# Optimization experiments

Hardware: AMD Instinct MI355X
Metric: run time of the kernel (lower is better)

The kernel has to match this reference:

```python
import jax, jax.numpy as jnp
import numpy as np

N_NODES = 20000
N_EDGES = 200000
NODE_DIM = 32
EDGE_DIM = 16
HIDDEN = 32
N_GRAPHS = 64


def setup_inputs() -> dict:
    key = jax.random.key(0)
    ks = jax.random.split(key, 20)
    x = jax.random.normal(ks[0], (N_NODES, NODE_DIM), jnp.float32)
    edge_attr = jax.random.normal(ks[1], (N_EDGES, EDGE_DIM), jnp.float32)
    edge_index = jax.random.randint(ks[2], (2, N_EDGES), 0, N_NODES, jnp.int64)
    batch = jnp.sort(jax.random.randint(ks[3], (N_NODES,), 0, N_GRAPHS, jnp.int64))
    s = 0.1
    # conv1 edge network: EDGE_DIM -> HIDDEN -> NODE_DIM*HIDDEN
    en1_W1 = jax.random.normal(ks[4], (EDGE_DIM, HIDDEN), jnp.float32) * s
    en1_b1 = jnp.zeros((HIDDEN,), jnp.float32)
    en1_W2 = jax.random.normal(ks[5], (HIDDEN, NODE_DIM * HIDDEN), jnp.float32) * s
    en1_b2 = jnp.zeros((NODE_DIM * HIDDEN,), jnp.float32)
    root1 = jax.random.normal(ks[6], (NODE_DIM, HIDDEN), jnp.float32) * s
    bias1 = jnp.zeros((HIDDEN,), jnp.float32)
    # conv2 edge network: EDGE_DIM -> HIDDEN -> HIDDEN*HIDDEN
    en2_W1 = jax.random.normal(ks[7], (EDGE_DIM, HIDDEN), jnp.float32) * s
    en2_b1 = jnp.zeros((HIDDEN,), jnp.float32)
    en2_W2 = jax.random.normal(ks[8], (HIDDEN, HIDDEN * HIDDEN), jnp.float32) * s
    en2_b2 = jnp.zeros((HIDDEN * HIDDEN,), jnp.float32)
    root2 = jax.random.normal(ks[9], (HIDDEN, HIDDEN), jnp.float32) * s
    bias2 = jnp.zeros((HIDDEN,), jnp.float32)
    # output head
    fc_W = jax.random.normal(ks[10], (HIDDEN, 2), jnp.float32) * s
    fc_b = jnp.zeros((2,), jnp.float32)
    return {
        "x": x, "edge_attr": edge_attr, "edge_index": edge_index, "batch": batch,
        "en1_W1": en1_W1, "en1_b1": en1_b1, "en1_W2": en1_W2, "en1_b2": en1_b2,
        "root1": root1, "bias1": bias1,
        "en2_W1": en2_W1, "en2_b1": en2_b1, "en2_W2": en2_W2, "en2_b2": en2_b2,
        "root2": root2, "bias2": bias2,
        "fc_W": fc_W, "fc_b": fc_b,
    }


def _segment_mean(vals, ids, num_segments):
    s = jax.ops.segment_sum(vals, ids, num_segments=num_segments)
    cnt = jax.ops.segment_sum(jnp.ones((vals.shape[0],), vals.dtype), ids, num_segments=num_segments)
    return s / jnp.maximum(cnt, 1.0)[:, None]


def _nnconv(x, src, tgt, edge_attr, W1, b1, W2, b2, root, bias, in_c, out_c, n_nodes):
    # edge MLP -> per-edge weight matrix [E, in_c, out_c]
    h = jax.nn.relu(edge_attr @ W1 + b1)
    Wedge = (h @ W2 + b2).reshape(-1, in_c, out_c)
    # gather source feats, per-edge matvec, scatter-mean to targets
    msg = jnp.einsum('ei,eio->eo', x[src], Wedge)
    agg = _segment_mean(msg, tgt, n_nodes)
    return agg + x @ root + bias


def reference(x, edge_attr, edge_index, batch,
              en1_W1, en1_b1, en1_W2, en1_b2, root1, bias1,
              en2_W1, en2_b1, en2_W2, en2_b2, root2, bias2,
              fc_W, fc_b):
    src, tgt = edge_index[0], edge_index[1]
    h = _nnconv(x, src, tgt, edge_attr, en1_W1, en1_b1, en1_W2, en1_b2,
                root1, bias1, NODE_DIM, HIDDEN, N_NODES)
    h = jax.nn.relu(h)
    h = _nnconv(h, src, tgt, edge_attr, en2_W1, en2_b1, en2_W2, en2_b2,
                root2, bias2, HIDDEN, HIDDEN, N_NODES)
    h = jax.nn.relu(h)
    g = _segment_mean(h, batch, N_GRAPHS)  # global_mean_pool
    return g @ fc_W + fc_b
```

## Files before the change

### kernel.cpp

```cpp
#include <hip/hip_runtime.h>

#define N_NODES   20000
#define N_EDGES   200000
#define NODE_DIM  32
#define EDGE_DIM  16
#define HIDDEN    32
#define N_GRAPHS  64
#define T_NODES   14


__global__ __launch_bounds__(256) void build_deg2_kernel(
    const int* __restrict__ tgts, const int* __restrict__ srcs,
    int* __restrict__ deg_t, int* __restrict__ deg_s)
{
    int e = blockIdx.x * blockDim.x + threadIdx.x;
    if (e >= N_EDGES) return;
    atomicAdd(deg_t + tgts[e], 1);
    atomicAdd(deg_s + srcs[e], 1);
}

__device__ void chunked_scan(const int* __restrict__ deg, int* __restrict__ start,
                             int* __restrict__ cursor, int* partial)
{
    const int C = (N_NODES + 255) / 256;
    int t  = threadIdx.x;
    int lo = t * C;
    int hi = lo + C < N_NODES ? lo + C : N_NODES;
    int s = 0;
    for (int i = lo; i < hi; ++i) s += deg[i];
    partial[t] = s;
    __syncthreads();
    if (t == 0) {
        int run = 0;
        for (int i = 0; i < 256; ++i) { int v = partial[i]; partial[i] = run; run += v; }
    }
    __syncthreads();
    int run = partial[t];
    for (int i = lo; i < hi; ++i) {
        start[i]  = run;
        cursor[i] = run;
        run += deg[i];
    }
    if (lo < N_NODES && hi == N_NODES) start[N_NODES] = run;
    __syncthreads();
}

__global__ __launch_bounds__(256) void scan2_kernel(
    const int* __restrict__ deg_t, int* __restrict__ start_t, int* __restrict__ cur_t,
    const int* __restrict__ deg_s, int* __restrict__ start_s, int* __restrict__ cur_s)
{
    __shared__ int partial[256];
    chunked_scan(deg_t, start_t, cur_t, partial);
    chunked_scan(deg_s, start_s, cur_s, partial);
}

__global__ __launch_bounds__(256) void scatter2_kernel(
    const int* __restrict__ tgts, const int* __restrict__ srcs,
    int* __restrict__ cur_t, int* __restrict__ cur_s,
    int* __restrict__ pos_t, int* __restrict__ eid_s)
{
    int e = blockIdx.x * blockDim.x + threadIdx.x;
    if (e >= N_EDGES) return;
    int p1 = atomicAdd(cur_t + tgts[e], 1);
    pos_t[e] = p1;
    int p2 = atomicAdd(cur_s + srcs[e], 1);
    eid_s[p2] = e;
}

__global__ __launch_bounds__(256, 2) void src_conv_kernel(
    const float* __restrict__ feat,
    const float* __restrict__ ea,
    const int*   __restrict__ srcs,
    const int*   __restrict__ start_s,
    const int*   __restrict__ eid_s,
    const int*   __restrict__ pos_t,
    const float* __restrict__ W1,
    const float* __restrict__ b1,
    const float* __restrict__ W2,
    const float* __restrict__ b2,
    float*       __restrict__ msg)
{
    __shared__ __align__(16) float P[T_NODES][1024];
    __shared__ __align__(16) float Q[T_NODES][32];
    __shared__ __align__(16) float XT[T_NODES][32];
    __shared__ __align__(16) float Hs[8][32];

    int tid = threadIdx.x;
    int v0  = blockIdx.x * T_NODES;
    int T_act = (N_NODES - v0) < T_NODES ? (N_NODES - v0) : T_NODES;

    if (tid < 8 * T_NODES) {
        int t  = tid >> 3;
        int og = tid & 7;
        int vv = v0 + t; if (vv > N_NODES - 1) vv = N_NODES - 1;
        float4 xx = *reinterpret_cast<const float4*>(feat + (size_t)vv * 32 + og * 4);
        *reinterpret_cast<float4*>(&XT[t][og * 4]) = xx;
    }
    __syncthreads();

    {
        int og = tid & 7;
        int k  = tid >> 3;
        float acc[T_NODES][4];
        #pragma unroll
        for (int t = 0; t < T_NODES; ++t) {
            acc[t][0] = 0.f; acc[t][1] = 0.f; acc[t][2] = 0.f; acc[t][3] = 0.f;
        }
        const float* w2p = W2 + (size_t)k * 1024 + og * 4;
        #pragma unroll
        for (int i = 0; i < 32; ++i) {
            float4 w4 = *reinterpret_cast<const float4*>(w2p + i * 32);
            #pragma unroll
            for (int t = 0; t < T_NODES; ++t) {
                float xv = XT[t][i];
                acc[t][0] += xv * w4.x; acc[t][1] += xv * w4.y;
                acc[t][2] += xv * w4.z; acc[t][3] += xv * w4.w;
            }
        }
        #pragma unroll
        for (int t = 0; t < T_NODES; ++t) {
            #pragma unroll
            for (int c = 0; c < 4; ++c) {
                int o = og * 4 + c;
                P[t][o * 32 + (k ^ ((o & 7) << 2))] = acc[t][c];
            }
        }
    }
    if (tid < 8 * T_NODES) {
        int t  = tid >> 3;
        int og = tid & 7;
        float q0 = 0.f, q1 = 0.f, q2 = 0.f, q3 = 0.f;
        const float* b2p = b2 + og * 4;
        #pragma unroll
        for (int i = 0; i < 32; ++i) {
            float4 b4 = *reinterpret_cast<const float4*>(b2p + i * 32);
            float xv = XT[t][i];
            q0 += xv * b4.x; q1 += xv * b4.y; q2 += xv * b4.z; q3 += xv * b4.w;
        }
        float4 qq; qq.x = q0; qq.y = q1; qq.z = q2; qq.w = q3;
        *reinterpret_cast<float4*>(&Q[t][og * 4]) = qq;
    }
    __syncthreads();

    int jb = start_s[v0];
    int je = start_s[v0 + T_act];
    int slot = tid >> 5;
    int kl   = tid & 31;
    int sw   = (kl & 7) << 2;

    float w1c[EDGE_DIM];
    #pragma unroll
    for (int j = 0; j < EDGE_DIM; ++j) w1c[j] = W1[j * 32 + kl];
    float b1v = b1[kl];

    for (int j0 = jb; j0 < je; j0 += 8) {
        int j = j0 + slot;
        if (j < je) {
            int e  = eid_s[j];
            int sl = srcs[e] - v0;
            int pr = pos_t[e];
            const float4* ea4 = reinterpret_cast<const float4*>(ea + (size_t)e * EDGE_DIM);
            float4 a0 = ea4[0], a1 = ea4[1], a2 = ea4[2], a3 = ea4[3];
            float hv = b1v;
            hv += a0.x * w1c[0]  + a0.y * w1c[1]  + a0.z * w1c[2]  + a0.w * w1c[3];
            hv += a1.x * w1c[4]  + a1.y * w1c[5]  + a1.z * w1c[6]  + a1.w * w1c[7];
            hv += a2.x * w1c[8]  + a2.y * w1c[9]  + a2.z * w1c[10] + a2.w * w1c[11];
            hv += a3.x * w1c[12] + a3.y * w1c[13] + a3.z * w1c[14] + a3.w * w1c[15];
            Hs[slot][kl] = fmaxf(hv, 0.f);

            float accv = Q[sl][kl];
            const float* Pt = &P[sl][kl * 32];
            #pragma unroll
            for (int kq = 0; kq < 32; kq += 4) {
                float4 hq = *reinterpret_cast<const float4*>(&Hs[slot][kq]);
                float4 pq = *reinterpret_cast<const float4*>(&Pt[kq ^ sw]);
                accv += hq.x * pq.x + hq.y * pq.y + hq.z * pq.z + hq.w * pq.w;
            }
            msg[(size_t)pr * 32 + kl] = accv;
        }
    }
}

__global__ __launch_bounds__(256, 2) void gather_update_kernel(
    const float* __restrict__ feat,
    const float* __restrict__ msg,
    const int*   __restrict__ start,
    const float* __restrict__ root,
    const float* __restrict__ bias,
    float*       __restrict__ outf,
    const int*   __restrict__ batch,
    float*       __restrict__ pool,
    float*       __restrict__ pcnt)
{
    int idx = blockIdx.x * blockDim.x + threadIdx.x;
    int v  = idx >> 3;
    int c4 = idx & 7;
    if (v >= N_NODES) return;

    int s0 = start[v], s1 = start[v + 1];
    const float4* m4 = reinterpret_cast<const float4*>(msg);

    float4 a0 = {0.f,0.f,0.f,0.f}, a1 = {0.f,0.f,0.f,0.f};
    float4 a2 = {0.f,0.f,0.f,0.f}, a3 = {0.f,0.f,0.f,0.f};
    int j = s0;
    for (; j + 4 <= s1; j += 4) {
        float4 t0 = m4[(size_t)(j + 0) * 8 + c4];
        float4 t1 = m4[(size_t)(j + 1) * 8 + c4];
        float4 t2 = m4[(size_t)(j + 2) * 8 + c4];
        float4 t3 = m4[(size_t)(j + 3) * 8 + c4];
        a0.x += t0.x; a0.y += t0.y; a0.z += t0.z; a0.w += t0.w;
        a1.x += t1.x; a1.y += t1.y; a1.z += t1.z; a1.w += t1.w;
        a2.x += t2.x; a2.y += t2.y; a2.z += t2.z; a2.w += t2.w;
        a3.x += t3.x; a3.y += t3.y; a3.z += t3.z; a3.w += t3.w;
    }
    for (; j < s1; ++j) {
        float4 t = m4[(size_t)j * 8 + c4];
        a0.x += t.x; a0.y += t.y; a0.z += t.z; a0.w += t.w;
    }
    float sx = (a0.x + a1.x) + (a2.x + a3.x);
    float sy = (a0.y + a1.y) + (a2.y + a3.y);
    float sz = (a0.z + a1.z) + (a2.z + a3.z);
    float sw_ = (a0.w + a1.w) + (a2.w + a3.w);

    int d = s1 - s0;
    float invd = 1.0f / (float)(d > 0 ? d : 1);
    float4 bb = *reinterpret_cast<const float4*>(bias + c4 * 4);
    float ax = sx * invd + bb.x;
    float ay = sy * invd + bb.y;
    float az = sz * invd + bb.z;
    float aw = sw_ * invd + bb.w;

    const float*  xv = feat + (size_t)v * 32;
    const float4* r4 = reinterpret_cast<const float4*>(root);
    #pragma unroll
    for (int i = 0; i < 32; ++i) {
        float  xi = xv[i];
        float4 rr = r4[i * 8 + c4];
        ax += xi * rr.x; ay += xi * rr.y; az += xi * rr.z; aw += xi * rr.w;
    }
    ax = fmaxf(ax, 0.f); ay = fmaxf(ay, 0.f); az = fmaxf(az, 0.f); aw = fmaxf(aw, 0.f);

    if (outf) {
        float4 t; t.x = ax; t.y = ay; t.z = az; t.w = aw;
        *reinterpret_cast<float4*>(outf + (size_t)v * 32 + c4 * 4) = t;
    }
    if (batch) {
        int g = batch[v];
        float* p = pool + (size_t)g * 32 + c4 * 4;
        atomicAdd(p + 0, ax); atomicAdd(p + 1, ay);
        atomicAdd(p + 2, az); atomicAdd(p + 3, aw);
        if (c4 == 0) atomicAdd(pcnt + g, 1.0f);
    }
}

__global__ void head_kernel(
    const float* __restrict__ pool, const float* __restrict__ pcnt,
    const float* __restrict__ fcW, const float* __restrict__ fcb,
    float* __restrict__ out)
{
    int g = threadIdx.x;
    if (g >= N_GRAPHS) return;
    float inv = 1.0f / fmaxf(pcnt[g], 1.0f);
    float o0 = fcb[0], o1 = fcb[1];
    #pragma unroll
    for (int i = 0; i < 32; ++i) {
        float m = pool[g * 32 + i] * inv;
        o0 += m * fcW[i * 2 + 0];
        o1 += m * fcW[i * 2 + 1];
    }
    out[g * 2 + 0] = o0;
    out[g * 2 + 1] = o1;
}

__global__ __launch_bounds__(256) void build_deg_kernel(
    const int* __restrict__ tgts, int* __restrict__ deg)
{
    int e = blockIdx.x * blockDim.x + threadIdx.x;
    if (e >= N_EDGES) return;
    atomicAdd(deg + tgts[e], 1);
}

__global__ __launch_bounds__(256) void scan_deg_kernel(
    const int* __restrict__ deg, int* __restrict__ start, int* __restrict__ cursor)
{
    __shared__ int partial[256];
    chunked_scan(deg, start, cursor, partial);
}

__global__ __launch_bounds__(256) void scatter_edges_kernel(
    const int* __restrict__ tgts, int* __restrict__ cursor, int* __restrict__ eid)
{
    int e = blockIdx.x * blockDim.x + threadIdx.x;
    if (e >= N_EDGES) return;
    int pos = atomicAdd(cursor + tgts[e], 1);
    eid[pos] = e;
}

__global__ __launch_bounds__(256) void edge_msg_kernel(
    const float* __restrict__ feat, const float* __restrict__ ea,
    const int* __restrict__ srcs,
    const float* __restrict__ W1, const float* __restrict__ b1,
    const float* __restrict__ W2, const float* __restrict__ b2,
    float* __restrict__ msg)
{
    int e = blockIdx.x * blockDim.x + threadIdx.x;
    if (e >= N_EDGES) return;
    float a[EDGE_DIM];
    const float4* ea4 = reinterpret_cast<const float4*>(ea + (size_t)e * EDGE_DIM);
    #pragma unroll
    for (int q = 0; q < EDGE_DIM / 4; ++q) {
        float4 t = ea4[q];
        a[q*4+0] = t.x; a[q*4+1] = t.y; a[q*4+2] = t.z; a[q*4+3] = t.w;
    }
    int s = srcs[e];
    float x[32];
    const float4* x4 = reinterpret_cast<const float4*>(feat + (size_t)s * 32);
    #pragma unroll
    for (int q = 0; q < 8; ++q) {
        float4 t = x4[q];
        x[q*4+0] = t.x; x[q*4+1] = t.y; x[q*4+2] = t.z; x[q*4+3] = t.w;
    }
    float acc[32];
    #pragma unroll
    for (int o = 0; o < 32; ++o) acc[o] = 0.0f;
    #pragma unroll
    for (int i = 0; i < 32; ++i) {
        float xi = x[i];
        #pragma unroll
        for (int o = 0; o < 32; ++o) acc[o] += xi * b2[i*32+o];
    }
    for (int k = 0; k < 32; ++k) {
        float hk = b1[k];
        #pragma unroll
        for (int j = 0; j < EDGE_DIM; ++j) hk += a[j] * W1[j*32 + k];
        hk = fmaxf(hk, 0.0f);
        const float* w = W2 + (size_t)k * 1024;
        #pragma unroll
        for (int i = 0; i < 32; ++i) {
            float c = hk * x[i];
            #pragma unroll
            for (int o = 0; o < 32; ++o) acc[o] += c * w[i*32+o];
        }
    }
    float4* m4 = reinterpret_cast<float4*>(msg + (size_t)e * 32);
    #pragma unroll
    for (int q = 0; q < 8; ++q) {
        float4 t;
        t.x = acc[q*4+0]; t.y = acc[q*4+1]; t.z = acc[q*4+2]; t.w = acc[q*4+3];
        m4[q] = t;
    }
}

__global__ __launch_bounds__(256) void gather_update_eid_kernel(
    const float* __restrict__ feat, const float* __restrict__ msg,
    const int* __restrict__ start, const int* __restrict__ eid,
    const float* __restrict__ root, const float* __restrict__ bias,
    float* __restrict__ outf, const int* __restrict__ batch,
    float* __restrict__ pool, float* __restrict__ pcnt)
{
    int idx = blockIdx.x * blockDim.x + threadIdx.x;
    int v = idx >> 5;
    int o = idx & 31;
    if (v >= N_NODES) return;
    int s0 = start[v], s1 = start[v + 1];
    float sum = 0.0f;
    for (int j = s0; j < s1; ++j) {
        int e = eid[j];
        sum += msg[(size_t)e * 32 + o];
    }
    int d = s1 - s0;
    float acc = sum / (float)(d > 0 ? d : 1) + bias[o];
    const float* xv = feat + (size_t)v * 32;
    #pragma unroll
    for (int i = 0; i < 32; ++i) acc += xv[i] * root[i * 32 + o];
    acc = fmaxf(acc, 0.0f);
    if (outf) outf[(size_t)v * 32 + o] = acc;
    if (batch) {
        int g = batch[v];
        atomicAdd(pool + (size_t)g * 32 + o, acc);
        if (o == 0) atomicAdd(pcnt + g, 1.0f);
    }
}


extern "C" void kernel_launch(void* const* d_in, const int* in_sizes, int n_in,
                              void* d_out, int out_size, void* d_ws, size_t ws_size,
                              hipStream_t stream)
{
    const float* x      = (const float*)d_in[0];
    const float* ea     = (const float*)d_in[1];
    const int*   ei     = (const int*)d_in[2];
    const int*   batch  = (const int*)d_in[3];
    const float* en1_W1 = (const float*)d_in[4];
    const float* en1_b1 = (const float*)d_in[5];
    const float* en1_W2 = (const float*)d_in[6];
    const float* en1_b2 = (const float*)d_in[7];
    const float* root1  = (const float*)d_in[8];
    const float* bias1  = (const float*)d_in[9];
    const float* en2_W1 = (const float*)d_in[10];
    const float* en2_b1 = (const float*)d_in[11];
    const float* en2_W2 = (const float*)d_in[12];
    const float* en2_b2 = (const float*)d_in[13];
    const float* root2  = (const float*)d_in[14];
    const float* bias2  = (const float*)d_in[15];
    const float* fcW    = (const float*)d_in[16];
    const float* fcb    = (const float*)d_in[17];

    const int* srcs = ei;
    const int* tgts = ei + N_EDGES;

    dim3 eb(256), eg((N_EDGES + 255) / 256);
    dim3 gb(256), gg((N_NODES * 8 + 255) / 256);
    const int NBLK = (N_NODES + T_NODES - 1) / T_NODES;

    size_t need_new = (size_t)2*N_NODES + N_GRAPHS*32 + N_GRAPHS
                    + 2*(N_NODES + 2) + 2*N_NODES + 2*(size_t)N_EDGES
                    + (size_t)N_EDGES*32 + (size_t)N_NODES*32;

    if (ws_size >= need_new * sizeof(float)) {
        int*   deg_t   = (int*)d_ws;
        int*   deg_s   = deg_t + N_NODES;
        float* pool    = (float*)(deg_s + N_NODES);
        float* pcnt    = pool + (size_t)N_GRAPHS*32;
        int*   start_t = (int*)(pcnt + N_GRAPHS);
        int*   cur_t   = start_t + (N_NODES + 2);
        int*   pos_t   = cur_t + N_NODES;
        int*   start_s = pos_t + N_EDGES;
        int*   cur_s   = start_s + (N_NODES + 2);
        int*   eid_s   = cur_s + N_NODES;
        float* msg     = (float*)(eid_s + N_EDGES);
        float* h1      = msg + (size_t)N_EDGES*32;
        size_t zeroBytes = ((size_t)2*N_NODES + N_GRAPHS*32 + N_GRAPHS) * sizeof(float);

        hipMemsetAsync(d_ws, 0, zeroBytes, stream);

        build_deg2_kernel<<<eg, eb, 0, stream>>>(tgts, srcs, deg_t, deg_s);
        scan2_kernel<<<dim3(1), dim3(256), 0, stream>>>(deg_t, start_t, cur_t,
                                                        deg_s, start_s, cur_s);
        scatter2_kernel<<<eg, eb, 0, stream>>>(tgts, srcs, cur_t, cur_s, pos_t, eid_s);

        src_conv_kernel<<<dim3(NBLK), dim3(256), 0, stream>>>(
            x, ea, srcs, start_s, eid_s, pos_t, en1_W1, en1_b1, en1_W2, en1_b2, msg);
        gather_update_kernel<<<gg, gb, 0, stream>>>(x, msg, start_t, root1, bias1,
                                                    h1, nullptr, nullptr, nullptr);
        src_conv_kernel<<<dim3(NBLK), dim3(256), 0, stream>>>(
            h1, ea, srcs, start_s, eid_s, pos_t, en2_W1, en2_b1, en2_W2, en2_b2, msg);
        gather_update_kernel<<<gg, gb, 0, stream>>>(h1, msg, start_t, root2, bias2,
                                                    nullptr, batch, pool, pcnt);

        head_kernel<<<dim3(1), dim3(64), 0, stream>>>(pool, pcnt, fcW, fcb, (float*)d_out);
    } else {
        int*   deg    = (int*)d_ws;
        float* pool   = (float*)(deg + N_NODES);
        float* pcnt   = pool + (size_t)N_GRAPHS*32;
        int*   start  = (int*)(pcnt + N_GRAPHS);
        int*   cursor = start + (N_NODES + 1);
        int*   eid    = cursor + N_NODES;
        float* msg    = (float*)(eid + N_EDGES);
        float* h1     = msg + (size_t)N_EDGES*32;
        size_t zeroBytes = ((size_t)N_NODES + N_GRAPHS*32 + N_GRAPHS) * sizeof(float);

        hipMemsetAsync(d_ws, 0, zeroBytes, stream);

        dim3 gg32((N_NODES * 32 + 255) / 256);
        build_deg_kernel<<<eg, eb, 0, stream>>>(tgts, deg);
        scan_deg_kernel<<<dim3(1), dim3(256), 0, stream>>>(deg, start, cursor);
        scatter_edges_kernel<<<eg, eb, 0, stream>>>(tgts, cursor, eid);

        edge_msg_kernel<<<eg, eb, 0, stream>>>(x, ea, srcs,
                                               en1_W1, en1_b1, en1_W2, en1_b2, msg);
        gather_update_eid_kernel<<<gg32, gb, 0, stream>>>(x, msg, start, eid, root1, bias1,
                                                          h1, nullptr, nullptr, nullptr);
        edge_msg_kernel<<<eg, eb, 0, stream>>>(h1, ea, srcs,
                                               en2_W1, en2_b1, en2_W2, en2_b2, msg);
        edge_msg_kernel<<<eg, eb, 0, stream>>>(h1, ea, srcs,
                                               en2_W1, en2_b1, en2_W2, en2_b2, msg);
        gather_update_eid_kernel<<<gg32, gb, 0, stream>>>(h1, msg, start, eid, root2, bias2,
                                                          nullptr, batch, pool, pcnt);
        head_kernel<<<dim3(1), dim3(64), 0, stream>>>(pool, pcnt, fcW, fcb, (float*)d_out);
    }
}
```

Before: 446.3 us.

## Balance the gather by edge-count blocks with shared-memory binning of messages

Replaces the per-node gather/update with an edge-balanced scheme. Blocks own a fixed span of target-sorted message rows, find their node range by binary search over start offsets, and accumulate rows into shared-memory bins with LDS atomics. Each row also records its target node in a new mapping array. The goal is to remove load imbalance from skewed in-degrees and to give coalesced row reads. The cost is an extra kernel, extra workspace, shared atomics and an uncoalesced per-thread root matvec.

Measured after the change: 508.4 us. 13.9% more time.

```diff
diff --git a/kernel.cpp b/kernel.cpp
--- a/kernel.cpp
+++ b/kernel.cpp
@@ -7,6 +7,9 @@
 #define HIDDEN    32
 #define N_GRAPHS  64
 #define T_NODES   14
+#define R_PER_BLK 512
+#define NCHUNK    128
+#define NB_GATHER ((N_EDGES + R_PER_BLK - 1) / R_PER_BLK)
 
 
 __global__ __launch_bounds__(256) void build_deg2_kernel(
@@ -57,28 +60,40 @@
 __global__ __launch_bounds__(256) void scatter2_kernel(
     const int* __restrict__ tgts, const int* __restrict__ srcs,
     int* __restrict__ cur_t, int* __restrict__ cur_s,
-    int* __restrict__ pos_t, int* __restrict__ eid_s)
+    int* __restrict__ pos_t, int* __restrict__ eid_s, int* __restrict__ r2n)
 {
     int e = blockIdx.x * blockDim.x + threadIdx.x;
     if (e >= N_EDGES) return;
-    int p1 = atomicAdd(cur_t + tgts[e], 1);
+    int t = tgts[e];
+    int p1 = atomicAdd(cur_t + t, 1);
     pos_t[e] = p1;
+    r2n[p1]  = t;
     int p2 = atomicAdd(cur_s + srcs[e], 1);
     eid_s[p2] = e;
 }
 
+__global__ __launch_bounds__(256) void find_block_starts_kernel(
+    const int* __restrict__ start_t, int* __restrict__ blk_first)
+{
+    int b = blockIdx.x * blockDim.x + threadIdx.x;
+    if (b > NB_GATHER) return;
+    int target = b * R_PER_BLK;
+    int lo = 0, hi = N_NODES + 1;
+    while (lo < hi) {
+        int mid = (lo + hi) >> 1;
+        if (start_t[mid] < target) lo = mid + 1; else hi = mid;
+    }
+    if (lo > N_NODES) lo = N_NODES;
+    blk_first[b] = lo;
+}
+
 __global__ __launch_bounds__(256, 2) void src_conv_kernel(
-    const float* __restrict__ feat,
-    const float* __restrict__ ea,
-    const int*   __restrict__ srcs,
-    const int*   __restrict__ start_s,
-    const int*   __restrict__ eid_s,
-    const int*   __restrict__ pos_t,
-    const float* __restrict__ W1,
-    const float* __restrict__ b1,
-    const float* __restrict__ W2,
-    const float* __restrict__ b2,
-    float*       __restrict__ msg)
+    const float* __restrict__ feat, const float* __restrict__ ea,
+    const int* __restrict__ srcs, const int* __restrict__ start_s,
+    const int* __restrict__ eid_s, const int* __restrict__ pos_t,
+    const float* __restrict__ W1, const float* __restrict__ b1,
+    const float* __restrict__ W2, const float* __restrict__ b2,
+    float* __restrict__ msg)
 {
     __shared__ __align__(16) float P[T_NODES][1024];
     __shared__ __align__(16) float Q[T_NODES][32];
@@ -181,10 +196,12 @@
     }
 }
 
-__global__ __launch_bounds__(256, 2) void gather_update_kernel(
+__global__ __launch_bounds__(256) void gather_block_kernel(
     const float* __restrict__ feat,
     const float* __restrict__ msg,
-    const int*   __restrict__ start,
+    const int*   __restrict__ start_t,
+    const int*   __restrict__ r2n,
+    const int*   __restrict__ blk_first,
     const float* __restrict__ root,
     const float* __restrict__ bias,
     float*       __restrict__ outf,
@@ -192,16 +209,93 @@
     float*       __restrict__ pool,
     float*       __restrict__ pcnt)
 {
+    __shared__ float bins[NCHUNK][32];
+
+    int b    = blockIdx.x;
+    int v_lo = blk_first[b];
+    int v_hi = blk_first[b + 1];
+    if (v_lo >= v_hi) return;
+
+    int tid  = threadIdx.x;
+    int slot = tid >> 5;
+    int o    = tid & 31;
+
+    for (int c_lo = v_lo; c_lo < v_hi; c_lo += NCHUNK) {
+        int c_hi = c_lo + NCHUNK < v_hi ? c_lo + NCHUNK : v_hi;
+
+        for (int i = tid; i < NCHUNK * 32; i += 256) ((float*)bins)[i] = 0.f;
+        __syncthreads();
+
+        int r_lo = start_t[c_lo];
+        int r_hi = start_t[c_hi];
+
+        for (int r0 = r_lo; r0 < r_hi; r0 += 32) {
+            int ra = r0 + slot, rb = ra + 8, rc = ra + 16, rd = ra + 24;
+            float va = 0.f, vb = 0.f, vc = 0.f, vd = 0.f;
+            int   na = 0, nb = 0, nc = 0, nd = 0;
+            bool  ga = ra < r_hi, gb = rb < r_hi, gc = rc < r_hi, gd = rd < r_hi;
+            if (ga) { va = msg[(size_t)ra * 32 + o]; na = r2n[ra]; }
+            if (gb) { vb = msg[(size_t)rb * 32 + o]; nb = r2n[rb]; }
+            if (gc) { vc = msg[(size_t)rc * 32 + o]; nc = r2n[rc]; }
+            if (gd) { vd = msg[(size_t)rd * 32 + o]; nd = r2n[rd]; }
+            if (ga) atomicAdd(&bins[na - c_lo][o], va);
+            if (gb) atomicAdd(&bins[nb - c_lo][o], vb);
+            if (gc) atomicAdd(&bins[nc - c_lo][o], vc);
+            if (gd) atomicAdd(&bins[nd - c_lo][o], vd);
+        }
+        __syncthreads();
+
+        for (int n = c_lo + slot; n < c_hi; n += 8) {
+            int d = start_t[n + 1] - start_t[n];
+            float acc = bins[n - c_lo][o] / (float)(d > 0 ? d : 1) + bias[o];
+            const float* xv = feat + (size_t)n * 32;
+            #pragma unroll
+            for (int i = 0; i < 32; ++i) acc += xv[i] * root[i * 32 + o];
+            acc = fmaxf(acc, 0.0f);
+            if (outf) outf[(size_t)n * 32 + o] = acc;
+            if (batch) {
+                int g = batch[n];
+                atomicAdd(pool + (size_t)g * 32 + o, acc);
+                if (o == 0) atomicAdd(pcnt + g, 1.0f);
+            }
+        }
+        __syncthreads();
+    }
+}
+
+__global__ void head_kernel(
+    const float* __restrict__ pool, const float* __restrict__ pcnt,
+    const float* __restrict__ fcW, const float* __restrict__ fcb,
+    float* __restrict__ out)
+{
+    int g = threadIdx.x;
+    if (g >= N_GRAPHS) return;
+    float inv = 1.0f / fmaxf(pcnt[g], 1.0f);
+    float o0 = fcb[0], o1 = fcb[1];
+    #pragma unroll
+    for (int i = 0; i < 32; ++i) {
+        float m = pool[g * 32 + i] * inv;
+        o0 += m * fcW[i * 2 + 0];
+        o1 += m * fcW[i * 2 + 1];
+    }
+    out[g * 2 + 0] = o0;
+    out[g * 2 + 1] = o1;
+}
+
+__global__ __launch_bounds__(256, 2) void gather_update_kernel(
+    const float* __restrict__ feat, const float* __restrict__ msg,
+    const int* __restrict__ start, const float* __restrict__ root,
+    const float* __restrict__ bias, float* __restrict__ outf,
+    const int* __restrict__ batch, float* __restrict__ pool,
+    float* __restrict__ pcnt)
+{
     int idx = blockIdx.x * blockDim.x + threadIdx.x;
     int v  = idx >> 3;
     int c4 = idx & 7;
     if (v >= N_NODES) return;
-
     int s0 = start[v], s1 = start[v + 1];
     const float4* m4 = reinterpret_cast<const float4*>(msg);
-
-    float4 a0 = {0.f,0.f,0.f,0.f}, a1 = {0.f,0.f,0.f,0.f};
-    float4 a2 = {0.f,0.f,0.f,0.f}, a3 = {0.f,0.f,0.f,0.f};
+    float4 a0 = {0,0,0,0}, a1 = {0,0,0,0}, a2 = {0,0,0,0}, a3 = {0,0,0,0};
     int j = s0;
     for (; j + 4 <= s1; j += 4) {
         float4 t0 = m4[(size_t)(j + 0) * 8 + c4];
@@ -221,15 +315,11 @@
     float sy = (a0.y + a1.y) + (a2.y + a3.y);
     float sz = (a0.z + a1.z) + (a2.z + a3.z);
     float sw_ = (a0.w + a1.w) + (a2.w + a3.w);
-
     int d = s1 - s0;
     float invd = 1.0f / (float)(d > 0 ? d : 1);
     float4 bb = *reinterpret_cast<const float4*>(bias + c4 * 4);
-    float ax = sx * invd + bb.x;
-    float ay = sy * invd + bb.y;
-    float az = sz * invd + bb.z;
-    float aw = sw_ * invd + bb.w;
-
+    float ax = sx * invd + bb.x, ay = sy * invd + bb.y;
+    float az = sz * invd + bb.z, aw = sw_ * invd + bb.w;
     const float*  xv = feat + (size_t)v * 32;
     const float4* r4 = reinterpret_cast<const float4*>(root);
     #pragma unroll
@@ -239,7 +329,6 @@
         ax += xi * rr.x; ay += xi * rr.y; az += xi * rr.z; aw += xi * rr.w;
     }
     ax = fmaxf(ax, 0.f); ay = fmaxf(ay, 0.f); az = fmaxf(az, 0.f); aw = fmaxf(aw, 0.f);
-
     if (outf) {
         float4 t; t.x = ax; t.y = ay; t.z = az; t.w = aw;
         *reinterpret_cast<float4*>(outf + (size_t)v * 32 + c4 * 4) = t;
@@ -251,25 +340,6 @@
         atomicAdd(p + 2, az); atomicAdd(p + 3, aw);
         if (c4 == 0) atomicAdd(pcnt + g, 1.0f);
     }
-}
-
-__global__ void head_kernel(
-    const float* __restrict__ pool, const float* __restrict__ pcnt,
-    const float* __restrict__ fcW, const float* __restrict__ fcb,
-    float* __restrict__ out)
-{
-    int g = threadIdx.x;
-    if (g >= N_GRAPHS) return;
-    float inv = 1.0f / fmaxf(pcnt[g], 1.0f);
-    float o0 = fcb[0], o1 = fcb[1];
-    #pragma unroll
-    for (int i = 0; i < 32; ++i) {
-        float m = pool[g * 32 + i] * inv;
-        o0 += m * fcW[i * 2 + 0];
-        o1 += m * fcW[i * 2 + 1];
-    }
-    out[g * 2 + 0] = o0;
-    out[g * 2 + 1] = o1;
 }
 
 __global__ __launch_bounds__(256) void build_deg_kernel(
@@ -410,14 +480,54 @@
     const int* tgts = ei + N_EDGES;
 
     dim3 eb(256), eg((N_EDGES + 255) / 256);
-    dim3 gb(256), gg((N_NODES * 8 + 255) / 256);
     const int NBLK = (N_NODES + T_NODES - 1) / T_NODES;
 
-    size_t need_new = (size_t)2*N_NODES + N_GRAPHS*32 + N_GRAPHS
-                    + 2*(N_NODES + 2) + 2*N_NODES + 2*(size_t)N_EDGES
-                    + (size_t)N_EDGES*32 + (size_t)N_NODES*32;
-
-    if (ws_size >= need_new * sizeof(float)) {
+    size_t base = (size_t)2*N_NODES + N_GRAPHS*32 + N_GRAPHS
+                + 2*(N_NODES + 2) + 2*N_NODES + 2*(size_t)N_EDGES
+                + (size_t)N_EDGES*32 + (size_t)N_NODES*32;
+    size_t need_v6 = base + N_EDGES + (NB_GATHER + 2);
+    size_t need_v5 = base;
+
+    if (ws_size >= need_v6 * sizeof(float)) {
+        int*   deg_t   = (int*)d_ws;
+        int*   deg_s   = deg_t + N_NODES;
+        float* pool    = (float*)(deg_s + N_NODES);
+        float* pcnt    = pool + (size_t)N_GRAPHS*32;
+        int*   start_t = (int*)(pcnt + N_GRAPHS);
+        int*   cur_t   = start_t + (N_NODES + 2);
+        int*   pos_t   = cur_t + N_NODES;
+        int*   start_s = pos_t + N_EDGES;
+        int*   cur_s   = start_s + (N_NODES + 2);
+        int*   eid_s   = cur_s + N_NODES;
+        float* msg     = (float*)(eid_s + N_EDGES);
+        float* h1      = msg + (size_t)N_EDGES*32;
+        int*   r2n     = (int*)(h1 + (size_t)N_NODES*32);
+        int*   blk_first = r2n + N_EDGES;
+        size_t zeroBytes = ((size_t)2*N_NODES + N_GRAPHS*32 + N_GRAPHS) * sizeof(float);
+
+        hipMemsetAsync(d_ws, 0, zeroBytes, stream);
+
+        build_deg2_kernel<<<eg, eb, 0, stream>>>(tgts, srcs, deg_t, deg_s);
+        scan2_kernel<<<dim3(1), dim3(256), 0, stream>>>(deg_t, start_t, cur_t,
+                                                        deg_s, start_s, cur_s);
+        scatter2_kernel<<<eg, eb, 0, stream>>>(tgts, srcs, cur_t, cur_s,
+                                               pos_t, eid_s, r2n);
+        find_block_starts_kernel<<<dim3((NB_GATHER + 256) / 256), dim3(256), 0, stream>>>(
+            start_t, blk_first);
+
+        src_conv_kernel<<<dim3(NBLK), dim3(256), 0, stream>>>(
+            x, ea, srcs, start_s, eid_s, pos_t, en1_W1, en1_b1, en1_W2, en1_b2, msg);
+        gather_block_kernel<<<dim3(NB_GATHER), dim3(256), 0, stream>>>(
+            x, msg, start_t, r2n, blk_first, root1, bias1,
+            h1, nullptr, nullptr, nullptr);
+        src_conv_kernel<<<dim3(NBLK), dim3(256), 0, stream>>>(
+            h1, ea, srcs, start_s, eid_s, pos_t, en2_W1, en2_b1, en2_W2, en2_b2, msg);
+        gather_block_kernel<<<dim3(NB_GATHER), dim3(256), 0, stream>>>(
+            h1, msg, start_t, r2n, blk_first, root2, bias2,
+            nullptr, batch, pool, pcnt);
+
+        head_kernel<<<dim3(1), dim3(64), 0, stream>>>(pool, pcnt, fcW, fcb, (float*)d_out);
+    } else if (ws_size >= need_v5 * sizeof(float)) {
         int*   deg_t   = (int*)d_ws;
         int*   deg_s   = deg_t + N_NODES;
         float* pool    = (float*)(deg_s + N_NODES);
@@ -433,21 +543,20 @@
         size_t zeroBytes = ((size_t)2*N_NODES + N_GRAPHS*32 + N_GRAPHS) * sizeof(float);
 
         hipMemsetAsync(d_ws, 0, zeroBytes, stream);
-
         build_deg2_kernel<<<eg, eb, 0, stream>>>(tgts, srcs, deg_t, deg_s);
         scan2_kernel<<<dim3(1), dim3(256), 0, stream>>>(deg_t, start_t, cur_t,
                                                         deg_s, start_s, cur_s);
-        scatter2_kernel<<<eg, eb, 0, stream>>>(tgts, srcs, cur_t, cur_s, pos_t, eid_s);
-
+        scatter2_kernel<<<eg, eb, 0, stream>>>(tgts, srcs, cur_t, cur_s,
+                                               pos_t, eid_s, pos_t);
+        dim3 gg((N_NODES * 8 + 255) / 256);
         src_conv_kernel<<<dim3(NBLK), dim3(256), 0, stream>>>(
             x, ea, srcs, start_s, eid_s, pos_t, en1_W1, en1_b1, en1_W2, en1_b2, msg);
-        gather_update_kernel<<<gg, gb, 0, stream>>>(x, msg, start_t, root1, bias1,
+        gather_update_kernel<<<gg, eb, 0, stream>>>(x, msg, start_t, root1, bias1,
                                                     h1, nullptr, nullptr, nullptr);
         src_conv_kernel<<<dim3(NBLK), dim3(256), 0, stream>>>(
             h1, ea, srcs, start_s, eid_s, pos_t, en2_W1, en2_b1, en2_W2, en2_b2, msg);
-        gather_update_kernel<<<gg, gb, 0, stream>>>(h1, msg, start_t, root2, bias2,
+        gather_update_kernel<<<gg, eb, 0, stream>>>(h1, msg, start_t, root2, bias2,
                                                     nullptr, batch, pool, pcnt);
-
         head_kernel<<<dim3(1), dim3(64), 0, stream>>>(pool, pcnt, fcW, fcb, (float*)d_out);
     } else {
         int*   deg    = (int*)d_ws;
@@ -461,21 +570,17 @@
         size_t zeroBytes = ((size_t)N_NODES + N_GRAPHS*32 + N_GRAPHS) * sizeof(float);
 
         hipMemsetAsync(d_ws, 0, zeroBytes, stream);
-
         dim3 gg32((N_NODES * 32 + 255) / 256);
         build_deg_kernel<<<eg, eb, 0, stream>>>(tgts, deg);
         scan_deg_kernel<<<dim3(1), dim3(256), 0, stream>>>(deg, start, cursor);
         scatter_edges_kernel<<<eg, eb, 0, stream>>>(tgts, cursor, eid);
-
         edge_msg_kernel<<<eg, eb, 0, stream>>>(x, ea, srcs,
                                                en1_W1, en1_b1, en1_W2, en1_b2, msg);
-        gather_update_eid_kernel<<<gg32, gb, 0, stream>>>(x, msg, start, eid, root1, bias1,
+        gather_update_eid_kernel<<<gg32, eb, 0, stream>>>(x, msg, start, eid, root1, bias1,
                                                           h1, nullptr, nullptr, nullptr);
         edge_msg_kernel<<<eg, eb, 0, stream>>>(h1, ea, srcs,
                                                en2_W1, en2_b1, en2_W2, en2_b2, msg);
-        edge_msg_kernel<<<eg, eb, 0, stream>>>(h1, ea, srcs,
-                                               en2_W1, en2_b1, en2_W2, en2_b2, msg);
-        gather_update_eid_kernel<<<gg32, gb, 0, stream>>>(h1, msg, start, eid, root2, bias2,
+        gather_update_eid_kernel<<<gg32, eb, 0, stream>>>(h1, msg, start, eid, root2, bias2,
                                                           nullptr, batch, pool, pcnt);
         head_kernel<<<dim3(1), dim3(64), 0, stream>>>(pool, pcnt, fcW, fcb, (float*)d_out);
     }
```
